# Optimization experiments

Hardware: AMD Instinct MI355X
Metric: run time of the kernel (lower is better)

The kernel has to match this reference:

```python
import jax, jax.numpy as jnp
import numpy as np

N = 50000          # total nodes in batch
E = 800000         # total edges (avg degree 16)
G = 512            # number of graphs in batch
H = 64             # hidden_channels
L = 5              # num_layers
C_IN = 1           # in_channels
NUM_CLASSES = 2
BN_EPS = 1e-5


def setup_inputs() -> dict:
    key = jax.random.key(0)
    ks = jax.random.split(key, 12)
    x = jax.random.normal(ks[0], (N, C_IN), dtype=jnp.float32)
    edge_index = jax.random.randint(ks[1], (2, E), 0, N, dtype=jnp.int64)
    batch = jnp.sort(jax.random.randint(ks[2], (N,), 0, G, dtype=jnp.int64))
    s = 0.1
    # GINConv MLP params: layer0 input is C_IN, layers 1..4 input is H
    w1_0 = jax.random.normal(ks[3], (C_IN, H), dtype=jnp.float32) * s
    w1_rest = jax.random.normal(ks[4], (L - 1, H, H), dtype=jnp.float32) * s
    b1 = jax.random.normal(ks[5], (L, H), dtype=jnp.float32) * s
    gamma_mlp = jnp.ones((L, H), dtype=jnp.float32)
    beta_mlp = jnp.zeros((L, H), dtype=jnp.float32)
    w2 = jax.random.normal(ks[6], (L, H, H), dtype=jnp.float32) * s
    b2 = jax.random.normal(ks[7], (L, H), dtype=jnp.float32) * s
    # outer per-layer BatchNorm (BasicGNN norm) params
    gamma = jnp.ones((L, H), dtype=jnp.float32)
    beta = jnp.zeros((L, H), dtype=jnp.float32)
    lin_w = jax.random.normal(ks[8], (C_IN + H * L, NUM_CLASSES), dtype=jnp.float32) * s
    lin_b = jnp.zeros((NUM_CLASSES,), dtype=jnp.float32)
    return dict(x=x, edge_index=edge_index, batch=batch, w1_0=w1_0,
                w1_rest=w1_rest, b1=b1, gamma_mlp=gamma_mlp, beta_mlp=beta_mlp,
                w2=w2, b2=b2, gamma=gamma, beta=beta, lin_w=lin_w, lin_b=lin_b)


def _bn(h, g, b):
    # training-mode batch norm over the node axis (biased variance, as torch)
    mu = h.mean(axis=0)
    var = h.var(axis=0)
    return (h - mu) * jax.lax.rsqrt(var + BN_EPS) * g + b


def _gin_backbone(x, src, dst, w1_0, w1_rest, b1, gm, bm, w2, b2, go, bo):
    h = x
    outs = []
    for l in range(L):  # fixed small layer count
        agg = jax.ops.segment_sum(h[src], dst, num_segments=N)  # sum_{j->i} h_j
        z = h + agg  # (1+eps)*h_i + agg, eps=0
        w1 = w1_0 if l == 0 else w1_rest[l - 1]
        z = z @ w1 + b1[l]
        z = jax.nn.relu(_bn(z, gm[l], bm[l]))   # MLP inner norm+act
        z = z @ w2[l] + b2[l]
        z = jax.nn.relu(_bn(z, go[l], bo[l]))   # BasicGNN norm+act (jk set)
        h = z
        outs.append(h)
    return jnp.concatenate(outs, axis=1)  # jk='cat' -> [N, H*L]


def reference(x, edge_index, batch, w1_0, w1_rest, b1, gamma_mlp, beta_mlp,
              w2, b2, gamma, beta, lin_w, lin_b):
    src, dst = edge_index[0], edge_index[1]
    node_desc = _gin_backbone(x, src, dst, w1_0, w1_rest, b1,
                              gamma_mlp, beta_mlp, w2, b2, gamma, beta)
    graph_desc = jax.ops.segment_sum(node_desc, batch, num_segments=G)  # [G, H*L]
    first_desc = jax.ops.segment_sum(x, batch, num_segments=G)          # [G, C_IN]
    gdesc = jnp.concatenate((first_desc, graph_desc), axis=1)           # [G, C_IN+H*L]
    # final dropout is identity in eval mode
    return gdesc @ lin_w + lin_b
```

## Files before the change

### kernel.cpp

```cpp
#include <hip/hip_runtime.h>

#define NN 50000
#define NE 800000
#define NG 512
#define HC 64
#define NL 5
#define GD_COLS 321
#define BN_EPS 1e-5f
#define DEG_CAP 64

#define SLICE 6250
#define ECHUNK 3125

typedef unsigned short bf16_t;
typedef unsigned int uiv4 __attribute__((ext_vector_type(4)));
typedef __attribute__((ext_vector_type(8))) short short8v;
typedef __attribute__((ext_vector_type(4))) float f32x4;
typedef __attribute__((ext_vector_type(4))) unsigned uint4v;

static __device__ __forceinline__ unsigned f2bfbits(float f) {
    unsigned u = __float_as_uint(f);
    return (u + 0x7FFFu + ((u >> 16) & 1u)) >> 16;
}
static __device__ __forceinline__ bf16_t f2bf(float f) { return (bf16_t)f2bfbits(f); }
static __device__ __forceinline__ float bf2f(bf16_t h) {
    return __uint_as_float(((unsigned)h) << 16);
}
static __device__ __forceinline__ float bflo(unsigned w) { return __uint_as_float(w << 16); }
static __device__ __forceinline__ float bfhi(unsigned w) {
    return __uint_as_float(w & 0xffff0000u);
}

static __device__ __forceinline__ void mfma_gemm_phase(
    const unsigned* zw, const unsigned* wsm, const float* __restrict__ bias,
    bf16_t* __restrict__ out, float* __restrict__ statsOut, float (*redS)[64],
    float (*redQ)[64], int r0, int t, int lane, int wid) {
    int l15 = lane & 15, l4 = lane >> 4;
    int tr = wid >> 1;
    int tc0 = (wid & 1) * 2;
    f32x4 d0 = {0.f, 0.f, 0.f, 0.f}, d1 = {0.f, 0.f, 0.f, 0.f};
    const unsigned* arow = &zw[(tr * 16 + l15) * 33];
    const unsigned* brow0 = &wsm[(tc0 * 16 + l15) * 33];
    const unsigned* brow1 = &wsm[((tc0 + 1) * 16 + l15) * 33];
#pragma unroll
    for (int kc = 0; kc < 2; ++kc) {
        int kb = kc * 16 + l4 * 4;
        uint4v aw = {arow[kb], arow[kb + 1], arow[kb + 2], arow[kb + 3]};
        uint4v bw0 = {brow0[kb], brow0[kb + 1], brow0[kb + 2], brow0[kb + 3]};
        uint4v bw1 = {brow1[kb], brow1[kb + 1], brow1[kb + 2], brow1[kb + 3]};
        short8v af = __builtin_bit_cast(short8v, aw);
        d0 = __builtin_amdgcn_mfma_f32_16x16x32_bf16(af, __builtin_bit_cast(short8v, bw0), d0,
                                                     0, 0, 0);
        d1 = __builtin_amdgcn_mfma_f32_16x16x32_bf16(af, __builtin_bit_cast(short8v, bw1), d1,
                                                     0, 0, 0);
    }
    int c0 = tc0 * 16 + l15, c1 = c0 + 16;
    float bv0 = bias[c0], bv1 = bias[c1];
    float s0 = 0.f, q0 = 0.f, s1 = 0.f, q1 = 0.f;
#pragma unroll
    for (int j = 0; j < 4; ++j) {
        int gr = r0 + tr * 16 + l4 * 4 + j;
        if (gr < NN) {
            float v0 = d0[j] + bv0, v1 = d1[j] + bv1;
            out[(size_t)gr * HC + c0] = f2bf(v0);
            out[(size_t)gr * HC + c1] = f2bf(v1);
            s0 += v0;
            q0 += v0 * v0;
            s1 += v1;
            q1 += v1 * v1;
        }
    }
    s0 += __shfl_xor(s0, 16); s0 += __shfl_xor(s0, 32);
    q0 += __shfl_xor(q0, 16); q0 += __shfl_xor(q0, 32);
    s1 += __shfl_xor(s1, 16); s1 += __shfl_xor(s1, 32);
    q1 += __shfl_xor(q1, 16); q1 += __shfl_xor(q1, 32);
    if (l4 == 0) { redS[wid][c0] = s0; redQ[wid][c0] = q0; }
    else if (l4 == 1) { redS[wid][c1] = s1; redQ[wid][c1] = q1; }
    else if (l4 == 2) { redS[wid][c0 ^ 32] = 0.f; redQ[wid][c0 ^ 32] = 0.f; }
    else { redS[wid][c1 ^ 32] = 0.f; redQ[wid][c1 ^ 32] = 0.f; }
    __syncthreads();
    if (t < 64) {
        float ts = 0.f, t2 = 0.f;
#pragma unroll
        for (int k = 0; k < 8; ++k) {
            ts += redS[k][t];
            t2 += redQ[k][t];
        }
        atomicAdd(&statsOut[t], ts);
        atomicAdd(&statsOut[64 + t], t2);
    }
}

__global__ __launch_bounds__(256) void scatter_kernel(const int* __restrict__ ei,
                                                      int* __restrict__ cnt,
                                                      unsigned short* __restrict__ ssrc,
                                                      float* __restrict__ stats,
                                                      float* __restrict__ gdesc) {
    int t = threadIdx.x;
    int g = blockIdx.x & 7;
    int c = blockIdx.x >> 3;
    int gt = blockIdx.x * 256 + t;
    int total = gridDim.x * 256;
    for (int i = gt; i < NL * 256; i += total) stats[i] = 0.f;
    for (int i = gt; i < NG * GD_COLS; i += total) gdesc[i] = 0.f;
    int lo = g * SLICE, hi = lo + SLICE;
    int e0 = c * ECHUNK;
    int e1 = e0 + ECHUNK;
    if (e1 > NE) e1 = NE;
    for (int e = e0 + t; e < e1; e += 256) {
        int d = ei[NE + e];
        if (d >= lo && d < hi) {
            int s = ei[e];
            int pos = atomicAdd(&cnt[d], 1);
            if (pos < DEG_CAP) ssrc[(d << 6) + pos] = (unsigned short)s;
        }
    }
}

__global__ __launch_bounds__(256) void layer0_kernel(
    const float* __restrict__ x, const int* __restrict__ cnt,
    const unsigned short* __restrict__ ssrc, const float* __restrict__ w,
    const float* __restrict__ bias, const int* __restrict__ batch, float* __restrict__ gdesc,
    bf16_t* __restrict__ y, float* __restrict__ stats) {
    __shared__ float z0p[256];
    __shared__ float z0s[64];
    int t = threadIdx.x, lane = t & 63, wid = t >> 6;
    int r0 = blockIdx.x * 64;
    if (t < 64) {
        int i = r0 + t;
        if (i < NN) atomicAdd(&gdesc[batch[i] * GD_COLS], x[i]);
    }
    {
        int node = t >> 2, sub = t & 3;
        int i = r0 + node;
        float acc = 0.f;
        if (i < NN) {
            int deg = cnt[i];
            if (deg > DEG_CAP) deg = DEG_CAP;
            int pa = i << 6;
            for (int p = sub; p < deg; p += 4) acc += x[ssrc[pa + p]];
            if (sub == 0) acc += x[i];
        }
        z0p[t] = acc;
    }
    __syncthreads();
    if (t < 64) z0s[t] = z0p[4 * t] + z0p[4 * t + 1] + z0p[4 * t + 2] + z0p[4 * t + 3];
    __syncthreads();
    float wv = w[lane], bv = bias[lane];
    float s = 0.f, s2 = 0.f;
    for (int j = 0; j < 16; ++j) {
        int r = r0 + wid * 16 + j;
        if (r < NN) {
            float v = z0s[wid * 16 + j] * wv + bv;
            y[r * HC + lane] = f2bf(v);
            s += v;
            s2 += v * v;
        }
    }
    __shared__ float ls[256], ls2[256];
    ls[t] = s;
    ls2[t] = s2;
    __syncthreads();
    if (wid == 0) {
        float ts = ls[lane] + ls[64 + lane] + ls[128 + lane] + ls[192 + lane];
        float t2 = ls2[lane] + ls2[64 + lane] + ls2[128 + lane] + ls2[192 + lane];
        atomicAdd(&stats[lane], ts);
        atomicAdd(&stats[64 + lane], t2);
    }
}

__global__ __launch_bounds__(512, 2) void gather_gemm_kernel(
    const bf16_t* __restrict__ u, const float* __restrict__ statsPrev,
    const float* __restrict__ gPrev, const float* __restrict__ bPrev,
    const int* __restrict__ cnt, const unsigned short* __restrict__ ssrc,
    const float* __restrict__ w, const float* __restrict__ bias, const int* __restrict__ batch,
    float* __restrict__ gdesc, int layerPrev, bf16_t* __restrict__ out,
    float* __restrict__ statsOut) {
    __shared__ unsigned zw[64 * 33];
    __shared__ unsigned wsm[64 * 33];
    __shared__ float a1[64], s1[64];
    __shared__ float redS[8][64], redQ[8][64];
    int t = threadIdx.x, lane = t & 63, wid = t >> 6;
    int r0 = blockIdx.x * 64;
    int li = lane & 7;
    int gq = lane >> 3;
    int gbase = lane & 56;
    int nB = r0 + wid * 8 + gq;
    uiv4 myidx;
    myidx[0] = 0; myidx[1] = 0; myidx[2] = 0; myidx[3] = 0;
    uiv4 selfv;
    selfv[0] = 0; selfv[1] = 0; selfv[2] = 0; selfv[3] = 0;
    int degB = 0;
    if (nB < NN) {
        degB = cnt[nB];
        if (degB > DEG_CAP) degB = DEG_CAP;
        myidx = *(const uiv4*)&ssrc[((size_t)nB << 6) + li * 8];
        selfv = *(const uiv4*)&u[(size_t)nB * HC + li * 8];
    }
    uiv4 rv0[8];
    {
        unsigned w0 = __shfl(myidx[0], gbase);
        unsigned w1 = __shfl(myidx[1], gbase);
        unsigned w2 = __shfl(myidx[2], gbase);
        unsigned w3 = __shfl(myidx[3], gbase);
        int id[8] = {(int)(w0 & 0xffff), (int)(w0 >> 16), (int)(w1 & 0xffff),
                     (int)(w1 >> 16),    (int)(w2 & 0xffff), (int)(w2 >> 16),
                     (int)(w3 & 0xffff), (int)(w3 >> 16)};
#pragma unroll
        for (int e = 0; e < 8; ++e)
            rv0[e] = *(const uiv4*)&u[(size_t)id[e] * HC + li * 8];
    }
    if (t < 64) {
        float mu = statsPrev[t] * (1.0f / NN);
        float var = statsPrev[64 + t] * (1.0f / NN) - mu * mu;
        float a = gPrev[t] * rsqrtf(var + BN_EPS);
        a1[t] = a;
        s1[t] = bPrev[t] - mu * a;
    }
    for (int idx = t; idx < 2048; idx += 512) {
        int kk = idx >> 6, c = idx & 63;
        unsigned lo = f2bfbits(w[(2 * kk) * 64 + c]);
        unsigned hi = f2bfbits(w[(2 * kk + 1) * 64 + c]);
        wsm[c * 33 + kk] = lo | (hi << 16);
    }
    __syncthreads();
    {
        float a8[8], s8[8];
#pragma unroll
        for (int c = 0; c < 8; ++c) {
            a8[c] = a1[li * 8 + c];
            s8[c] = s1[li * 8 + c];
        }
        float acc[8];
        if (nB < NN) {
            acc[0] = fmaxf(bflo(selfv[0]) * a8[0] + s8[0], 0.f);
            acc[1] = fmaxf(bfhi(selfv[0]) * a8[1] + s8[1], 0.f);
            acc[2] = fmaxf(bflo(selfv[1]) * a8[2] + s8[2], 0.f);
            acc[3] = fmaxf(bfhi(selfv[1]) * a8[3] + s8[3], 0.f);
            acc[4] = fmaxf(bflo(selfv[2]) * a8[4] + s8[4], 0.f);
            acc[5] = fmaxf(bfhi(selfv[2]) * a8[5] + s8[5], 0.f);
            acc[6] = fmaxf(bflo(selfv[3]) * a8[6] + s8[6], 0.f);
            acc[7] = fmaxf(bfhi(selfv[3]) * a8[7] + s8[7], 0.f);
        } else {
#pragma unroll
            for (int c = 0; c < 8; ++c) acc[c] = 0.f;
        }
        if (degB > 0) {
            uiv4 rv[8];
#pragma unroll
            for (int e = 0; e < 8; ++e) rv[e] = rv0[e];
            int cntA = degB < 8 ? degB : 8;
            for (int b = 1; cntA > 0; ++b) {
                uiv4 nv[8];
                int cntB = 0;
                if (b * 8 < degB) {
                    unsigned w0 = __shfl(myidx[0], gbase + b);
                    unsigned w1 = __shfl(myidx[1], gbase + b);
                    unsigned w2 = __shfl(myidx[2], gbase + b);
                    unsigned w3 = __shfl(myidx[3], gbase + b);
                    int id[8] = {(int)(w0 & 0xffff), (int)(w0 >> 16), (int)(w1 & 0xffff),
                                 (int)(w1 >> 16),    (int)(w2 & 0xffff), (int)(w2 >> 16),
                                 (int)(w3 & 0xffff), (int)(w3 >> 16)};
#pragma unroll
                    for (int e = 0; e < 8; ++e)
                        nv[e] = *(const uiv4*)&u[(size_t)id[e] * HC + li * 8];
                    cntB = degB - b * 8;
                    if (cntB > 8) cntB = 8;
                }
#pragma unroll
                for (int e = 0; e < 8; ++e) {
                    float v0 = fmaxf(bflo(rv[e][0]) * a8[0] + s8[0], 0.f);
                    float v1 = fmaxf(bfhi(rv[e][0]) * a8[1] + s8[1], 0.f);
                    float v2 = fmaxf(bflo(rv[e][1]) * a8[2] + s8[2], 0.f);
                    float v3 = fmaxf(bfhi(rv[e][1]) * a8[3] + s8[3], 0.f);
                    float v4 = fmaxf(bflo(rv[e][2]) * a8[4] + s8[4], 0.f);
                    float v5 = fmaxf(bfhi(rv[e][2]) * a8[5] + s8[5], 0.f);
                    float v6 = fmaxf(bflo(rv[e][3]) * a8[6] + s8[6], 0.f);
                    float v7 = fmaxf(bfhi(rv[e][3]) * a8[7] + s8[7], 0.f);
                    if (e < cntA) {
                        acc[0] += v0;
                        acc[1] += v1;
                        acc[2] += v2;
                        acc[3] += v3;
                        acc[4] += v4;
                        acc[5] += v5;
                        acc[6] += v6;
                        acc[7] += v7;
                    }
                }
#pragma unroll
                for (int e = 0; e < 8; ++e) rv[e] = nv[e];
                cntA = cntB;
            }
        }
        int lr = wid * 8 + gq;
        unsigned* zp = &zw[lr * 33 + li * 4];
        zp[0] = f2bfbits(acc[0]) | (f2bfbits(acc[1]) << 16);
        zp[1] = f2bfbits(acc[2]) | (f2bfbits(acc[3]) << 16);
        zp[2] = f2bfbits(acc[4]) | (f2bfbits(acc[5]) << 16);
        zp[3] = f2bfbits(acc[6]) | (f2bfbits(acc[7]) << 16);
    }
    {
        float av = a1[lane], sv = s1[lane];
        int col = 1 + layerPrev * HC + lane;
        float gacc = 0.f;
        int cur = -1;
        for (int j = 0; j < 8; ++j) {
            int gr = r0 + wid * 8 + j;
            if (gr < NN) {
                float hv = fmaxf(bf2f(u[(size_t)gr * HC + lane]) * av + sv, 0.f);
                int gid = batch[gr];
                if (gid != cur) {
                    if (cur >= 0) atomicAdd(&gdesc[cur * GD_COLS + col], gacc);
                    cur = gid;
                    gacc = 0.f;
                }
                gacc += hv;
            }
        }
        if (cur >= 0) atomicAdd(&gdesc[cur * GD_COLS + col], gacc);
    }
    __syncthreads();
    mfma_gemm_phase(zw, wsm, bias, out, statsOut, redS, redQ, r0, t, lane, wid);
}

__global__ __launch_bounds__(512) void gemm128_norm_kernel(
    const bf16_t* __restrict__ in, const float* __restrict__ w, const float* __restrict__ bias,
    const float* __restrict__ statsIn, const float* __restrict__ gIn,
    const float* __restrict__ bIn, bf16_t* __restrict__ out, float* __restrict__ statsOut) {
    __shared__ unsigned zw[128 * 33];
    __shared__ unsigned wsm[64 * 33];
    __shared__ float a1[64], s1[64];
    __shared__ float redS[8][64], redQ[8][64];
    int t = threadIdx.x, lane = t & 63, wid = t >> 6;
    int r0 = blockIdx.x * 128;
    if (t < 64) {
        float mu = statsIn[t] * (1.0f / NN);
        float var = statsIn[64 + t] * (1.0f / NN) - mu * mu;
        float a = gIn[t] * rsqrtf(var + BN_EPS);
        a1[t] = a;
        s1[t] = bIn[t] - mu * a;
    }
    for (int idx = t; idx < 2048; idx += 512) {
        int kk = idx >> 6, c = idx & 63;
        unsigned lo = f2bfbits(w[(2 * kk) * 64 + c]);
        unsigned hi = f2bfbits(w[(2 * kk + 1) * 64 + c]);
        wsm[c * 33 + kk] = lo | (hi << 16);
    }
    __syncthreads();
    for (int idx = t; idx < 4096; idx += 512) {
        int r = idx >> 5, kk = idx & 31;
        int gr = r0 + r;
        unsigned zword = 0u;
        if (gr < NN) {
            unsigned word = *(const unsigned*)&in[(size_t)gr * HC + 2 * kk];
            float v0 = fmaxf(bflo(word) * a1[2 * kk] + s1[2 * kk], 0.f);
            float v1 = fmaxf(bfhi(word) * a1[2 * kk + 1] + s1[2 * kk + 1], 0.f);
            zword = f2bfbits(v0) | (f2bfbits(v1) << 16);
        }
        zw[r * 33 + kk] = zword;
    }
    __syncthreads();
    int l15 = lane & 15, l4 = lane >> 4;
    const unsigned* arow = &zw[(wid * 16 + l15) * 33];
    f32x4 d[4];
#pragma unroll
    for (int tc = 0; tc < 4; ++tc) d[tc] = (f32x4){0.f, 0.f, 0.f, 0.f};
#pragma unroll
    for (int kc = 0; kc < 2; ++kc) {
        int kb = kc * 16 + l4 * 4;
        uint4v aw = {arow[kb], arow[kb + 1], arow[kb + 2], arow[kb + 3]};
        short8v af = __builtin_bit_cast(short8v, aw);
#pragma unroll
        for (int tc = 0; tc < 4; ++tc) {
            const unsigned* brow = &wsm[(tc * 16 + l15) * 33];
            uint4v bw = {brow[kb], brow[kb + 1], brow[kb + 2], brow[kb + 3]};
            d[tc] = __builtin_amdgcn_mfma_f32_16x16x32_bf16(af, __builtin_bit_cast(short8v, bw),
                                                            d[tc], 0, 0, 0);
        }
    }
    float ss[4], qq[4];
#pragma unroll
    for (int tc = 0; tc < 4; ++tc) {
        int cc = tc * 16 + l15;
        float bv = bias[cc];
        float s = 0.f, q = 0.f;
#pragma unroll
        for (int j = 0; j < 4; ++j) {
            int gr = r0 + wid * 16 + l4 * 4 + j;
            if (gr < NN) {
                float v = d[tc][j] + bv;
                out[(size_t)gr * HC + cc] = f2bf(v);
                s += v;
                q += v * v;
            }
        }
        s += __shfl_xor(s, 16); s += __shfl_xor(s, 32);
        q += __shfl_xor(q, 16); q += __shfl_xor(q, 32);
        ss[tc] = s;
        qq[tc] = q;
    }
    if (lane < 16) {
#pragma unroll
        for (int tc = 0; tc < 4; ++tc) {
            redS[wid][tc * 16 + lane] = ss[tc];
            redQ[wid][tc * 16 + lane] = qq[tc];
        }
    }
    __syncthreads();
    if (t < 64) {
        float ts = 0.f, t2 = 0.f;
#pragma unroll
        for (int k = 0; k < 8; ++k) {
            ts += redS[k][t];
            t2 += redQ[k][t];
        }
        atomicAdd(&statsOut[t], ts);
        atomicAdd(&statsOut[64 + t], t2);
    }
}

#define CHK 16
__global__ void gdesc_last_kernel(const bf16_t* __restrict__ u, const float* __restrict__ stats,
                                  const float* __restrict__ g, const float* __restrict__ b,
                                  const int* __restrict__ batch, float* __restrict__ gdesc,
                                  int layer) {
    int lane = threadIdx.x & 63;
    int wid = threadIdx.x >> 6;
    int i0 = (blockIdx.x * 4 + wid) * CHK;
    if (i0 >= NN) return;
    float mu = stats[lane] * (1.0f / NN);
    float var = stats[64 + lane] * (1.0f / NN) - mu * mu;
    float a = g[lane] * rsqrtf(var + BN_EPS);
    float s = b[lane] - mu * a;
    int col = 1 + layer * HC + lane;
    float acc = 0.f;
    int cur = -1;
    int iend = i0 + CHK;
    if (iend > NN) iend = NN;
    for (int i = i0; i < iend; ++i) {
        int gid = batch[i];
        if (gid != cur) {
            if (cur >= 0) atomicAdd(&gdesc[cur * GD_COLS + col], acc);
            cur = gid;
            acc = 0.f;
        }
        acc += fmaxf(bf2f(u[i * HC + lane]) * a + s, 0.f);
    }
    if (cur >= 0) atomicAdd(&gdesc[cur * GD_COLS + col], acc);
}

__global__ void final_gemm_kernel(const float* __restrict__ gdesc, const float* __restrict__ lw,
                                  const float* __restrict__ lb, float* __restrict__ out) {
    int g = blockIdx.x;
    int lane = threadIdx.x;
    float a0 = 0.f, a1 = 0.f;
    for (int j = lane; j < GD_COLS; j += 64) {
        float v = gdesc[g * GD_COLS + j];
        a0 += v * lw[j * 2 + 0];
        a1 += v * lw[j * 2 + 1];
    }
    for (int off = 32; off > 0; off >>= 1) {
        a0 += __shfl_down(a0, off);
        a1 += __shfl_down(a1, off);
    }
    if (lane == 0) {
        out[g * 2 + 0] = a0 + lb[0];
        out[g * 2 + 1] = a1 + lb[1];
    }
}

extern "C" void kernel_launch(void* const* d_in, const int* in_sizes, int n_in, void* d_out,
                              int out_size, void* d_ws, size_t ws_size, hipStream_t stream) {
    const float* x = (const float*)d_in[0];
    const int* ei = (const int*)d_in[1];
    const int* batch = (const int*)d_in[2];
    const float* w1_0 = (const float*)d_in[3];
    const float* w1_rest = (const float*)d_in[4];
    const float* b1 = (const float*)d_in[5];
    const float* gm = (const float*)d_in[6];
    const float* bm = (const float*)d_in[7];
    const float* w2 = (const float*)d_in[8];
    const float* b2 = (const float*)d_in[9];
    const float* go = (const float*)d_in[10];
    const float* bo = (const float*)d_in[11];
    const float* lw = (const float*)d_in[12];
    const float* lb = (const float*)d_in[13];
    float* out = (float*)d_out;

    float* stats = (float*)d_ws;
    float* gdesc = stats + NL * 256;
    bf16_t* ybuf = (bf16_t*)(gdesc + (size_t)NG * GD_COLS + 64);
    bf16_t* ubuf = ybuf + (size_t)NN * HC;
    int* cnt = (int*)(ubuf + (size_t)NN * HC);
    unsigned short* ssrc = (unsigned short*)(cnt + NN);

    hipMemsetAsync(cnt, 0, NN * sizeof(int), stream);

    scatter_kernel<<<2048, 256, 0, stream>>>(ei, cnt, ssrc, stats, gdesc);

    layer0_kernel<<<(NN + 63) / 64, 256, 0, stream>>>(x, cnt, ssrc, w1_0, b1, batch, gdesc, ybuf,
                                                      stats);
    gemm128_norm_kernel<<<(NN + 127) / 128, 512, 0, stream>>>(ybuf, w2, b2, stats, gm, bm, ubuf,
                                                              stats + 128);
    for (int l = 1; l < NL; ++l) {
        float* st1 = stats + l * 256;
        float* st2 = st1 + 128;
        float* stPrev = stats + (l - 1) * 256 + 128;
        gather_gemm_kernel<<<(NN + 63) / 64, 512, 0, stream>>>(
            ubuf, stPrev, go + (l - 1) * HC, bo + (l - 1) * HC, cnt, ssrc,
            w1_rest + (size_t)(l - 1) * HC * HC, b1 + l * HC, batch, gdesc, l - 1, ybuf, st1);
        gemm128_norm_kernel<<<(NN + 127) / 128, 512, 0, stream>>>(
            ybuf, w2 + (size_t)l * HC * HC, b2 + l * HC, st1, gm + l * HC, bm + l * HC, ubuf, st2);
    }
    gdesc_last_kernel<<<(NN + 4 * CHK - 1) / (4 * CHK), 256, 0, stream>>>(
        ubuf, stats + 4 * 256 + 128, go + 4 * HC, bo + 4 * HC, batch, gdesc, 4);
    final_gemm_kernel<<<NG, 64, 0, stream>>>(gdesc, lw, lb, out);
}
```

Measured before the change: 410.6 us.

## Halve gather_gemm block size so each wave gathers two nodes per lane group

The gather+GEMM kernel drops from 512 to 256 threads per block while keeping 64 rows per block. Each 8-lane group now gathers two nodes in sequence through a shared helper, and each wave computes a full 16x64 MFMA tile instead of a 16x32 half tile. This cuts the per-block reduction array and weight-loading parallelism and raises the occupancy hint to 3 blocks per CU. The trade is more serialized gather latency per wave, since only the first node's first neighbor batch is prefetched before the barrier, in return for more work per wave and fewer waves per block.

Measured after the change: 436.1 us. +6.2%, slower.

```diff
diff --git a/kernel.cpp b/kernel.cpp
--- a/kernel.cpp
+++ b/kernel.cpp
@@ -29,66 +29,6 @@
 static __device__ __forceinline__ float bflo(unsigned w) { return __uint_as_float(w << 16); }
 static __device__ __forceinline__ float bfhi(unsigned w) {
     return __uint_as_float(w & 0xffff0000u);
-}
-
-static __device__ __forceinline__ void mfma_gemm_phase(
-    const unsigned* zw, const unsigned* wsm, const float* __restrict__ bias,
-    bf16_t* __restrict__ out, float* __restrict__ statsOut, float (*redS)[64],
-    float (*redQ)[64], int r0, int t, int lane, int wid) {
-    int l15 = lane & 15, l4 = lane >> 4;
-    int tr = wid >> 1;
-    int tc0 = (wid & 1) * 2;
-    f32x4 d0 = {0.f, 0.f, 0.f, 0.f}, d1 = {0.f, 0.f, 0.f, 0.f};
-    const unsigned* arow = &zw[(tr * 16 + l15) * 33];
-    const unsigned* brow0 = &wsm[(tc0 * 16 + l15) * 33];
-    const unsigned* brow1 = &wsm[((tc0 + 1) * 16 + l15) * 33];
-#pragma unroll
-    for (int kc = 0; kc < 2; ++kc) {
-        int kb = kc * 16 + l4 * 4;
-        uint4v aw = {arow[kb], arow[kb + 1], arow[kb + 2], arow[kb + 3]};
-        uint4v bw0 = {brow0[kb], brow0[kb + 1], brow0[kb + 2], brow0[kb + 3]};
-        uint4v bw1 = {brow1[kb], brow1[kb + 1], brow1[kb + 2], brow1[kb + 3]};
-        short8v af = __builtin_bit_cast(short8v, aw);
-        d0 = __builtin_amdgcn_mfma_f32_16x16x32_bf16(af, __builtin_bit_cast(short8v, bw0), d0,
-                                                     0, 0, 0);
-        d1 = __builtin_amdgcn_mfma_f32_16x16x32_bf16(af, __builtin_bit_cast(short8v, bw1), d1,
-                                                     0, 0, 0);
-    }
-    int c0 = tc0 * 16 + l15, c1 = c0 + 16;
-    float bv0 = bias[c0], bv1 = bias[c1];
-    float s0 = 0.f, q0 = 0.f, s1 = 0.f, q1 = 0.f;
-#pragma unroll
-    for (int j = 0; j < 4; ++j) {
-        int gr = r0 + tr * 16 + l4 * 4 + j;
-        if (gr < NN) {
-            float v0 = d0[j] + bv0, v1 = d1[j] + bv1;
-            out[(size_t)gr * HC + c0] = f2bf(v0);
-            out[(size_t)gr * HC + c1] = f2bf(v1);
-            s0 += v0;
-            q0 += v0 * v0;
-            s1 += v1;
-            q1 += v1 * v1;
-        }
-    }
-    s0 += __shfl_xor(s0, 16); s0 += __shfl_xor(s0, 32);
-    q0 += __shfl_xor(q0, 16); q0 += __shfl_xor(q0, 32);
-    s1 += __shfl_xor(s1, 16); s1 += __shfl_xor(s1, 32);
-    q1 += __shfl_xor(q1, 16); q1 += __shfl_xor(q1, 32);
-    if (l4 == 0) { redS[wid][c0] = s0; redQ[wid][c0] = q0; }
-    else if (l4 == 1) { redS[wid][c1] = s1; redQ[wid][c1] = q1; }
-    else if (l4 == 2) { redS[wid][c0 ^ 32] = 0.f; redQ[wid][c0 ^ 32] = 0.f; }
-    else { redS[wid][c1 ^ 32] = 0.f; redQ[wid][c1 ^ 32] = 0.f; }
-    __syncthreads();
-    if (t < 64) {
-        float ts = 0.f, t2 = 0.f;
-#pragma unroll
-        for (int k = 0; k < 8; ++k) {
-            ts += redS[k][t];
-            t2 += redQ[k][t];
-        }
-        atomicAdd(&statsOut[t], ts);
-        atomicAdd(&statsOut[64 + t], t2);
-    }
 }
 
 __global__ __launch_bounds__(256) void scatter_kernel(const int* __restrict__ ei,
@@ -169,7 +109,91 @@
     }
 }
 
-__global__ __launch_bounds__(512, 2) void gather_gemm_kernel(
+static __device__ __forceinline__ void gather_accum(
+    const bf16_t* __restrict__ u, uiv4 myidx, uiv4 selfv, int deg, bool valid, int gbase,
+    int li, const float* a8, const float* s8, const uiv4* rv0pre, unsigned* zrow) {
+    float acc[8];
+    if (valid) {
+        acc[0] = fmaxf(bflo(selfv[0]) * a8[0] + s8[0], 0.f);
+        acc[1] = fmaxf(bfhi(selfv[0]) * a8[1] + s8[1], 0.f);
+        acc[2] = fmaxf(bflo(selfv[1]) * a8[2] + s8[2], 0.f);
+        acc[3] = fmaxf(bfhi(selfv[1]) * a8[3] + s8[3], 0.f);
+        acc[4] = fmaxf(bflo(selfv[2]) * a8[4] + s8[4], 0.f);
+        acc[5] = fmaxf(bfhi(selfv[2]) * a8[5] + s8[5], 0.f);
+        acc[6] = fmaxf(bflo(selfv[3]) * a8[6] + s8[6], 0.f);
+        acc[7] = fmaxf(bfhi(selfv[3]) * a8[7] + s8[7], 0.f);
+    } else {
+#pragma unroll
+        for (int c = 0; c < 8; ++c) acc[c] = 0.f;
+    }
+    if (deg > 0) {
+        uiv4 rv[8];
+        if (rv0pre) {
+#pragma unroll
+            for (int e = 0; e < 8; ++e) rv[e] = rv0pre[e];
+        } else {
+            unsigned w0 = __shfl(myidx[0], gbase);
+            unsigned w1 = __shfl(myidx[1], gbase);
+            unsigned w2 = __shfl(myidx[2], gbase);
+            unsigned w3 = __shfl(myidx[3], gbase);
+            int id[8] = {(int)(w0 & 0xffff), (int)(w0 >> 16), (int)(w1 & 0xffff),
+                         (int)(w1 >> 16),    (int)(w2 & 0xffff), (int)(w2 >> 16),
+                         (int)(w3 & 0xffff), (int)(w3 >> 16)};
+#pragma unroll
+            for (int e = 0; e < 8; ++e)
+                rv[e] = *(const uiv4*)&u[(size_t)id[e] * HC + li * 8];
+        }
+        int cntA = deg < 8 ? deg : 8;
+        for (int b = 1; cntA > 0; ++b) {
+            uiv4 nv[8];
+            int cntB = 0;
+            if (b * 8 < deg) {
+                unsigned w0 = __shfl(myidx[0], gbase + b);
+                unsigned w1 = __shfl(myidx[1], gbase + b);
+                unsigned w2 = __shfl(myidx[2], gbase + b);
+                unsigned w3 = __shfl(myidx[3], gbase + b);
+                int id[8] = {(int)(w0 & 0xffff), (int)(w0 >> 16), (int)(w1 & 0xffff),
+                             (int)(w1 >> 16),    (int)(w2 & 0xffff), (int)(w2 >> 16),
+                             (int)(w3 & 0xffff), (int)(w3 >> 16)};
+#pragma unroll
+                for (int e = 0; e < 8; ++e)
+                    nv[e] = *(const uiv4*)&u[(size_t)id[e] * HC + li * 8];
+                cntB = deg - b * 8;
+                if (cntB > 8) cntB = 8;
+            }
+#pragma unroll
+            for (int e = 0; e < 8; ++e) {
+                float v0 = fmaxf(bflo(rv[e][0]) * a8[0] + s8[0], 0.f);
+                float v1 = fmaxf(bfhi(rv[e][0]) * a8[1] + s8[1], 0.f);
+                float v2 = fmaxf(bflo(rv[e][1]) * a8[2] + s8[2], 0.f);
+                float v3 = fmaxf(bfhi(rv[e][1]) * a8[3] + s8[3], 0.f);
+                float v4 = fmaxf(bflo(rv[e][2]) * a8[4] + s8[4], 0.f);
+                float v5 = fmaxf(bfhi(rv[e][2]) * a8[5] + s8[5], 0.f);
+                float v6 = fmaxf(bflo(rv[e][3]) * a8[6] + s8[6], 0.f);
+                float v7 = fmaxf(bfhi(rv[e][3]) * a8[7] + s8[7], 0.f);
+                if (e < cntA) {
+                    acc[0] += v0;
+                    acc[1] += v1;
+                    acc[2] += v2;
+                    acc[3] += v3;
+                    acc[4] += v4;
+                    acc[5] += v5;
+                    acc[6] += v6;
+                    acc[7] += v7;
+                }
+            }
+#pragma unroll
+            for (int e = 0; e < 8; ++e) rv[e] = nv[e];
+            cntA = cntB;
+        }
+    }
+    zrow[0] = f2bfbits(acc[0]) | (f2bfbits(acc[1]) << 16);
+    zrow[1] = f2bfbits(acc[2]) | (f2bfbits(acc[3]) << 16);
+    zrow[2] = f2bfbits(acc[4]) | (f2bfbits(acc[5]) << 16);
+    zrow[3] = f2bfbits(acc[6]) | (f2bfbits(acc[7]) << 16);
+}
+
+__global__ __launch_bounds__(256, 3) void gather_gemm_kernel(
     const bf16_t* __restrict__ u, const float* __restrict__ statsPrev,
     const float* __restrict__ gPrev, const float* __restrict__ bPrev,
     const int* __restrict__ cnt, const unsigned short* __restrict__ ssrc,
@@ -179,30 +203,35 @@
     __shared__ unsigned zw[64 * 33];
     __shared__ unsigned wsm[64 * 33];
     __shared__ float a1[64], s1[64];
-    __shared__ float redS[8][64], redQ[8][64];
+    __shared__ float redS[4][64], redQ[4][64];
     int t = threadIdx.x, lane = t & 63, wid = t >> 6;
     int r0 = blockIdx.x * 64;
     int li = lane & 7;
     int gq = lane >> 3;
     int gbase = lane & 56;
-    int nB = r0 + wid * 8 + gq;
-    uiv4 myidx;
-    myidx[0] = 0; myidx[1] = 0; myidx[2] = 0; myidx[3] = 0;
-    uiv4 selfv;
-    selfv[0] = 0; selfv[1] = 0; selfv[2] = 0; selfv[3] = 0;
-    int degB = 0;
-    if (nB < NN) {
-        degB = cnt[nB];
-        if (degB > DEG_CAP) degB = DEG_CAP;
-        myidx = *(const uiv4*)&ssrc[((size_t)nB << 6) + li * 8];
-        selfv = *(const uiv4*)&u[(size_t)nB * HC + li * 8];
+    int n0 = r0 + wid * 16 + gq;
+    int n1 = n0 + 8;
+    uiv4 myidx0 = {0, 0, 0, 0}, myidx1 = {0, 0, 0, 0};
+    uiv4 selfv0 = {0, 0, 0, 0}, selfv1 = {0, 0, 0, 0};
+    int deg0 = 0, deg1 = 0;
+    if (n0 < NN) {
+        deg0 = cnt[n0];
+        if (deg0 > DEG_CAP) deg0 = DEG_CAP;
+        myidx0 = *(const uiv4*)&ssrc[((size_t)n0 << 6) + li * 8];
+        selfv0 = *(const uiv4*)&u[(size_t)n0 * HC + li * 8];
+    }
+    if (n1 < NN) {
+        deg1 = cnt[n1];
+        if (deg1 > DEG_CAP) deg1 = DEG_CAP;
+        myidx1 = *(const uiv4*)&ssrc[((size_t)n1 << 6) + li * 8];
+        selfv1 = *(const uiv4*)&u[(size_t)n1 * HC + li * 8];
     }
     uiv4 rv0[8];
     {
-        unsigned w0 = __shfl(myidx[0], gbase);
-        unsigned w1 = __shfl(myidx[1], gbase);
-        unsigned w2 = __shfl(myidx[2], gbase);
-        unsigned w3 = __shfl(myidx[3], gbase);
+        unsigned w0 = __shfl(myidx0[0], gbase);
+        unsigned w1 = __shfl(myidx0[1], gbase);
+        unsigned w2 = __shfl(myidx0[2], gbase);
+        unsigned w3 = __shfl(myidx0[3], gbase);
         int id[8] = {(int)(w0 & 0xffff), (int)(w0 >> 16), (int)(w1 & 0xffff),
                      (int)(w1 >> 16),    (int)(w2 & 0xffff), (int)(w2 >> 16),
                      (int)(w3 & 0xffff), (int)(w3 >> 16)};
@@ -217,7 +246,7 @@
         a1[t] = a;
         s1[t] = bPrev[t] - mu * a;
     }
-    for (int idx = t; idx < 2048; idx += 512) {
+    for (int idx = t; idx < 2048; idx += 256) {
         int kk = idx >> 6, c = idx & 63;
         unsigned lo = f2bfbits(w[(2 * kk) * 64 + c]);
         unsigned hi = f2bfbits(w[(2 * kk + 1) * 64 + c]);
@@ -231,82 +260,18 @@
             a8[c] = a1[li * 8 + c];
             s8[c] = s1[li * 8 + c];
         }
-        float acc[8];
-        if (nB < NN) {
-            acc[0] = fmaxf(bflo(selfv[0]) * a8[0] + s8[0], 0.f);
-            acc[1] = fmaxf(bfhi(selfv[0]) * a8[1] + s8[1], 0.f);
-            acc[2] = fmaxf(bflo(selfv[1]) * a8[2] + s8[2], 0.f);
-            acc[3] = fmaxf(bfhi(selfv[1]) * a8[3] + s8[3], 0.f);
-            acc[4] = fmaxf(bflo(selfv[2]) * a8[4] + s8[4], 0.f);
-            acc[5] = fmaxf(bfhi(selfv[2]) * a8[5] + s8[5], 0.f);
-            acc[6] = fmaxf(bflo(selfv[3]) * a8[6] + s8[6], 0.f);
-            acc[7] = fmaxf(bfhi(selfv[3]) * a8[7] + s8[7], 0.f);
-        } else {
-#pragma unroll
-            for (int c = 0; c < 8; ++c) acc[c] = 0.f;
-        }
-        if (degB > 0) {
-            uiv4 rv[8];
-#pragma unroll
-            for (int e = 0; e < 8; ++e) rv[e] = rv0[e];
-            int cntA = degB < 8 ? degB : 8;
-            for (int b = 1; cntA > 0; ++b) {
-                uiv4 nv[8];
-                int cntB = 0;
-                if (b * 8 < degB) {
-                    unsigned w0 = __shfl(myidx[0], gbase + b);
-                    unsigned w1 = __shfl(myidx[1], gbase + b);
-                    unsigned w2 = __shfl(myidx[2], gbase + b);
-                    unsigned w3 = __shfl(myidx[3], gbase + b);
-                    int id[8] = {(int)(w0 & 0xffff), (int)(w0 >> 16), (int)(w1 & 0xffff),
-                                 (int)(w1 >> 16),    (int)(w2 & 0xffff), (int)(w2 >> 16),
-                                 (int)(w3 & 0xffff), (int)(w3 >> 16)};
-#pragma unroll
-                    for (int e = 0; e < 8; ++e)
-                        nv[e] = *(const uiv4*)&u[(size_t)id[e] * HC + li * 8];
-                    cntB = degB - b * 8;
-                    if (cntB > 8) cntB = 8;
-                }
-#pragma unroll
-                for (int e = 0; e < 8; ++e) {
-                    float v0 = fmaxf(bflo(rv[e][0]) * a8[0] + s8[0], 0.f);
-                    float v1 = fmaxf(bfhi(rv[e][0]) * a8[1] + s8[1], 0.f);
-                    float v2 = fmaxf(bflo(rv[e][1]) * a8[2] + s8[2], 0.f);
-                    float v3 = fmaxf(bfhi(rv[e][1]) * a8[3] + s8[3], 0.f);
-                    float v4 = fmaxf(bflo(rv[e][2]) * a8[4] + s8[4], 0.f);
-                    float v5 = fmaxf(bfhi(rv[e][2]) * a8[5] + s8[5], 0.f);
-                    float v6 = fmaxf(bflo(rv[e][3]) * a8[6] + s8[6], 0.f);
-                    float v7 = fmaxf(bfhi(rv[e][3]) * a8[7] + s8[7], 0.f);
-                    if (e < cntA) {
-                        acc[0] += v0;
-                        acc[1] += v1;
-                        acc[2] += v2;
-                        acc[3] += v3;
-                        acc[4] += v4;
-                        acc[5] += v5;
-                        acc[6] += v6;
-                        acc[7] += v7;
-                    }
-                }
-#pragma unroll
-                for (int e = 0; e < 8; ++e) rv[e] = nv[e];
-                cntA = cntB;
-            }
-        }
-        int lr = wid * 8 + gq;
-        unsigned* zp = &zw[lr * 33 + li * 4];
-        zp[0] = f2bfbits(acc[0]) | (f2bfbits(acc[1]) << 16);
-        zp[1] = f2bfbits(acc[2]) | (f2bfbits(acc[3]) << 16);
-        zp[2] = f2bfbits(acc[4]) | (f2bfbits(acc[5]) << 16);
-        zp[3] = f2bfbits(acc[6]) | (f2bfbits(acc[7]) << 16);
+        gather_accum(u, myidx0, selfv0, deg0, n0 < NN, gbase, li, a8, s8, rv0,
+                     &zw[(wid * 16 + gq) * 33 + li * 4]);
+        gather_accum(u, myidx1, selfv1, deg1, n1 < NN, gbase, li, a8, s8, nullptr,
+                     &zw[(wid * 16 + 8 + gq) * 33 + li * 4]);
     }
     {
         float av = a1[lane], sv = s1[lane];
         int col = 1 + layerPrev * HC + lane;
         float gacc = 0.f;
         int cur = -1;
-        for (int j = 0; j < 8; ++j) {
-            int gr = r0 + wid * 8 + j;
+        for (int j = 0; j < 16; ++j) {
+            int gr = r0 + wid * 16 + j;
             if (gr < NN) {
                 float hv = fmaxf(bf2f(u[(size_t)gr * HC + lane]) * av + sv, 0.f);
                 int gid = batch[gr];
@@ -321,7 +286,63 @@
         if (cur >= 0) atomicAdd(&gdesc[cur * GD_COLS + col], gacc);
     }
     __syncthreads();
-    mfma_gemm_phase(zw, wsm, bias, out, statsOut, redS, redQ, r0, t, lane, wid);
+    int l15 = lane & 15, l4 = lane >> 4;
+    const unsigned* arow = &zw[(wid * 16 + l15) * 33];
+    f32x4 d[4];
+#pragma unroll
+    for (int tc = 0; tc < 4; ++tc) d[tc] = (f32x4){0.f, 0.f, 0.f, 0.f};
+#pragma unroll
+    for (int kc = 0; kc < 2; ++kc) {
+        int kb = kc * 16 + l4 * 4;
+        uint4v aw = {arow[kb], arow[kb + 1], arow[kb + 2], arow[kb + 3]};
+        short8v af = __builtin_bit_cast(short8v, aw);
+#pragma unroll
+        for (int tc = 0; tc < 4; ++tc) {
+            const unsigned* brow = &wsm[(tc * 16 + l15) * 33];
+            uint4v bw = {brow[kb], brow[kb + 1], brow[kb + 2], brow[kb + 3]};
+            d[tc] = __builtin_amdgcn_mfma_f32_16x16x32_bf16(af, __builtin_bit_cast(short8v, bw),
+                                                            d[tc], 0, 0, 0);
+        }
+    }
+    float ss[4], qq[4];
+#pragma unroll
+    for (int tc = 0; tc < 4; ++tc) {
+        int cc = tc * 16 + l15;
+        float bv = bias[cc];
+        float s = 0.f, q = 0.f;
+#pragma unroll
+        for (int j = 0; j < 4; ++j) {
+            int gr = r0 + wid * 16 + l4 * 4 + j;
+            if (gr < NN) {
+                float v = d[tc][j] + bv;
+                out[(size_t)gr * HC + cc] = f2bf(v);
+                s += v;
+                q += v * v;
+            }
+        }
+        s += __shfl_xor(s, 16); s += __shfl_xor(s, 32);
+        q += __shfl_xor(q, 16); q += __shfl_xor(q, 32);
+        ss[tc] = s;
+        qq[tc] = q;
+    }
+    if (lane < 16) {
+#pragma unroll
+        for (int tc = 0; tc < 4; ++tc) {
+            redS[wid][tc * 16 + lane] = ss[tc];
+            redQ[wid][tc * 16 + lane] = qq[tc];
+        }
+    }
+    __syncthreads();
+    if (t < 64) {
+        float ts = 0.f, t2 = 0.f;
+#pragma unroll
+        for (int k = 0; k < 4; ++k) {
+            ts += redS[k][t];
+            t2 += redQ[k][t];
+        }
+        atomicAdd(&statsOut[t], ts);
+        atomicAdd(&statsOut[64 + t], t2);
+    }
 }
 
 __global__ __launch_bounds__(512) void gemm128_norm_kernel(
@@ -507,7 +528,7 @@
         float* st1 = stats + l * 256;
         float* st2 = st1 + 128;
         float* stPrev = stats + (l - 1) * 256 + 128;
-        gather_gemm_kernel<<<(NN + 63) / 64, 512, 0, stream>>>(
+        gather_gemm_kernel<<<(NN + 63) / 64, 256, 0, stream>>>(
             ubuf, stPrev, go + (l - 1) * HC, bo + (l - 1) * HC, cnt, ssrc,
             w1_rest + (size_t)(l - 1) * HC * HC, b1 + l * HC, batch, gdesc, l - 1, ybuf, st1);
         gemm128_norm_kernel<<<(NN + 127) / 128, 512, 0, stream>>>(
```
